# Performance work log

Measured on AMD Instinct MI355X. Metric: run time of the kernel, lower is better.

The kernel has to match this reference:

```python
import jax, jax.numpy as jnp
import numpy as np

B, T, D, H = 4, 2048, 1024, 8
d = D // H
EPS = 1e-12  # torch F.normalize eps


def _l2norm(x):
    n = jnp.sqrt(jnp.sum(x * x, axis=-1, keepdims=True))
    return x / jnp.maximum(n, EPS)


def setup_inputs() -> dict:
    key = jax.random.key(0)
    ks = jax.random.split(key, 7)
    s = 1.0 / np.sqrt(D)
    return {
        "x": jax.random.normal(ks[0], (B, T, D), dtype=jnp.float32),
        "Wq": jax.random.uniform(ks[1], (D, D), jnp.float32, -s, s),
        "Wk": jax.random.uniform(ks[2], (D, D), jnp.float32, -s, s),
        "Wv": jax.random.uniform(ks[3], (D, D), jnp.float32, -s, s),
        "Wo": jax.random.uniform(ks[4], (D, D), jnp.float32, -s, s),
        "Wlr": jax.random.uniform(ks[5], (D, D), jnp.float32, -s, s),
        "b_lr": jnp.zeros((D,), jnp.float32),
    }


def reference(x, Wq, Wk, Wv, Wo, Wlr, b_lr):
    # projections (torch Linear: y = x @ W.T)
    q = (x @ Wq.T).reshape(B, T, H, d)
    k = _l2norm((x @ Wk.T).reshape(B, T, H, d))
    v = _l2norm((x @ Wv.T).reshape(B, T, H, d))
    lr = jax.nn.sigmoid(x @ Wlr.T + b_lr).reshape(B, T, H, d)

    # scan over time; state w: [B,H,d,d]
    def step(w, qkvl):
        q_t, k_t, v_t, lr_t = qkvl  # each [B,H,d]
        v_old = jnp.einsum('bhij,bhj->bhi', w, k_t)          # retrieve
        w = w + (lr_t * (v_t - v_old))[..., :, None] * k_t[..., None, :]
        o_t = jnp.einsum('bhij,bhj->bhi', w, q_t)            # read
        return w, o_t

    to_t = lambda a: jnp.moveaxis(a, 1, 0)  # [B,T,H,d] -> [T,B,H,d]
    w0 = jnp.zeros((B, H, d, d), dtype=q.dtype)
    _, o = jax.lax.scan(step, w0, (to_t(q), to_t(k), to_t(v), to_t(lr)))
    o = jnp.moveaxis(o, 0, 1).reshape(B, T, D)
    return o @ Wo.T
```

## Files before the change

### kernel.cpp

```cpp
#include <hip/hip_runtime.h>
#include <math.h>

#define Bsz  4
#define Tlen 2048
#define Dm   1024
#define Hh   8
#define dh   128
#define Mrows (Bsz * Tlen)

typedef __attribute__((ext_vector_type(8))) short  s16x8;
typedef __attribute__((ext_vector_type(4))) float  f32x4;

#define DPP_ADD(x, ctrl) \
    ((x) + __int_as_float(__builtin_amdgcn_update_dpp( \
        0, __float_as_int(x), (ctrl), 0xf, 0xf, true)))

__device__ inline unsigned short f2b_rne(float f) {
    unsigned int u = __float_as_uint(f);
    u += 0x7FFFu + ((u >> 16) & 1u);
    return (unsigned short)(u >> 16);
}

__global__ __launch_bounds__(256) void cvt_f32_bf16(const float* __restrict__ in,
                                                    unsigned short* __restrict__ out)
{
    const size_t i = ((size_t)blockIdx.x * 256 + threadIdx.x) * 4;
    float4 v = *(const float4*)&in[i];
    ushort4 o;
    o.x = f2b_rne(v.x); o.y = f2b_rne(v.y);
    o.z = f2b_rne(v.z); o.w = f2b_rne(v.w);
    *(ushort4*)&out[i] = o;
}

__global__ __launch_bounds__(256) void gemm_bf16(const unsigned short* __restrict__ A,
                                                 const unsigned short* __restrict__ Wt,
                                                 const float* __restrict__ bias,
                                                 float* __restrict__ Y,
                                                 int mode)
{
    __shared__ __align__(16) unsigned short As[128 * 32];
    __shared__ __align__(16) unsigned short Bs[128 * 32];

    const int tid   = threadIdx.x;
    const int w     = tid >> 6;
    const int lane  = tid & 63;
    const int r4    = lane >> 2;
    const int p4    = lane & 3;
    const int row16 = lane & 15;
    const int quad  = lane >> 4;

    const int m0 = blockIdx.y * 128;
    const int n0 = blockIdx.x * 128;
    const int wm = (w >> 1) * 64;
    const int wn = (w & 1) * 64;

    f32x4 acc[4][4];
#pragma unroll
    for (int i = 0; i < 4; ++i)
#pragma unroll
        for (int j = 0; j < 4; ++j)
            acc[i][j] = (f32x4){0.f, 0.f, 0.f, 0.f};

    for (int k0 = 0; k0 < 1024; k0 += 32) {
        __syncthreads();
#pragma unroll
        for (int c = 0; c < 2; ++c) {
            const int ml  = w * 32 + c * 16 + r4;
            const int swz = (ml >> 1) & 3;
            const unsigned short* ga = A  + (size_t)(m0 + ml) * 1024 + k0 + ((p4 ^ swz) << 3);
            const unsigned short* gb = Wt + (size_t)(n0 + ml) * 1024 + k0 + ((p4 ^ swz) << 3);
            __builtin_amdgcn_global_load_lds(
                (const __attribute__((address_space(1))) void*)ga,
                (__attribute__((address_space(3))) void*)&As[(w * 32 + c * 16) * 32], 16, 0, 0);
            __builtin_amdgcn_global_load_lds(
                (const __attribute__((address_space(1))) void*)gb,
                (__attribute__((address_space(3))) void*)&Bs[(w * 32 + c * 16) * 32], 16, 0, 0);
        }
        __syncthreads();

        s16x8 af[4], bf[4];
#pragma unroll
        for (int bm = 0; bm < 4; ++bm) {
            const int ml  = wm + bm * 16 + row16;
            const int pos = quad ^ ((ml >> 1) & 3);
            af[bm] = *(const s16x8*)&As[ml * 32 + pos * 8];
        }
#pragma unroll
        for (int bn = 0; bn < 4; ++bn) {
            const int nl  = wn + bn * 16 + row16;
            const int pos = quad ^ ((nl >> 1) & 3);
            bf[bn] = *(const s16x8*)&Bs[nl * 32 + pos * 8];
        }
#pragma unroll
        for (int bm = 0; bm < 4; ++bm)
#pragma unroll
            for (int bn = 0; bn < 4; ++bn)
                acc[bm][bn] = __builtin_amdgcn_mfma_f32_16x16x32_bf16(af[bm], bf[bn], acc[bm][bn], 0, 0, 0);
    }

#pragma unroll
    for (int bm = 0; bm < 4; ++bm) {
        const int row = m0 + wm + bm * 16 + quad * 4;
#pragma unroll
        for (int bn = 0; bn < 4; ++bn) {
            const int col = n0 + wn + bn * 16 + row16;
            const float bb = bias ? bias[col] : 0.f;
#pragma unroll
            for (int r = 0; r < 4; ++r) {
                float val = acc[bm][bn][r] + bb;
                if (mode == 1) val = 1.f / (1.f + __expf(-val));
                Y[(size_t)(row + r) * 1024 + col] = val;
            }
        }
    }
}

__global__ __launch_bounds__(256) void l2norm_kq(float* __restrict__ Kb,
                                                 float* __restrict__ Vb,
                                                 const float* __restrict__ Qb,
                                                 float* __restrict__ KQ)
{
    const int gtid = blockIdx.x * 256 + threadIdx.x;
    const int row  = gtid >> 6;
    const int lane = threadIdx.x & 63;
    const size_t base = (size_t)row * dh + lane * 2;

    float2 k2 = *(float2*)&Kb[base];
    float2 v2 = *(float2*)&Vb[base];
    float2 q2 = *(const float2*)&Qb[base];
    float sk = k2.x * k2.x + k2.y * k2.y;
    float sv = v2.x * v2.x + v2.y * v2.y;
    float sq = k2.x * q2.x + k2.y * q2.y;
#pragma unroll
    for (int off = 1; off < 64; off <<= 1) {
        sk += __shfl_xor(sk, off);
        sv += __shfl_xor(sv, off);
        sq += __shfl_xor(sq, off);
    }
    const float rk = 1.f / fmaxf(sqrtf(sk), 1e-12f);
    const float rv = 1.f / fmaxf(sqrtf(sv), 1e-12f);
    k2.x *= rk; k2.y *= rk;
    v2.x *= rv; v2.y *= rv;
    *(float2*)&Kb[base] = k2;
    *(float2*)&Vb[base] = v2;
    if (lane == 0) {
        const int b = row / (Tlen * Hh);
        const int t = (row / Hh) % Tlen;
        const int h = row % Hh;
        KQ[(size_t)(b * Hh + h) * Tlen + t] = sq * rk;
    }
}

__global__ __launch_bounds__(64) void scan_kernel(const float* __restrict__ Q,
                                                  const float* __restrict__ Kb,
                                                  const float* __restrict__ Vb,
                                                  const float* __restrict__ LR,
                                                  const float* __restrict__ KQ,
                                                  unsigned short* __restrict__ Obb)
{
    const int bid = blockIdx.x;
    const int bh  = bid & 31;
    const int rg  = bid >> 5;
    const int b   = bh >> 3, h = bh & 7;
    const int lane = threadIdx.x;
    const int rl   = lane >> 4;
    const int c16  = lane & 15;
    const int row  = rg * 4 + rl;

    const size_t base = (size_t)b * Tlen * Dm + (size_t)h * dh;
    const float* kp  = Kb + base + c16 * 8;
    const float* qp  = Q  + base + c16 * 8;
    const float* vp  = Vb + base + row;
    const float* lp  = LR + base + row;
    const float* kqp = KQ + (size_t)(b * Hh + h) * Tlen;
    unsigned short* op = Obb + base + row;

    float w[8];
#pragma unroll
    for (int i = 0; i < 8; ++i) w[i] = 0.f;

    float4 kr[8][2], qr[8][2];
    float  vv[8], lv[8], kqv[8];
#pragma unroll
    for (int u = 0; u < 8; ++u) {
        const size_t off = (size_t)u * Dm;
        kr[u][0] = *(const float4*)(kp + off);
        kr[u][1] = *(const float4*)(kp + off + 4);
        qr[u][0] = *(const float4*)(qp + off);
        qr[u][1] = *(const float4*)(qp + off + 4);
        vv[u] = vp[off];
        lv[u] = lp[off];
        kqv[u] = kqp[u];
    }

    float o8[8];

    for (int t = 0; t < Tlen; t += 8) {
#pragma unroll
        for (int u = 0; u < 8; ++u) {
            const int tc = t + u;
            const float4 ka = kr[u][0], kb = kr[u][1];
            const float4 qa = qr[u][0], qb = qr[u][1];
            const float vr = vv[u], lrr = lv[u], kq = kqv[u];

            int tn = tc + 8; if (tn >= Tlen) tn = Tlen - 1;
            const size_t offn = (size_t)tn * Dm;
            kr[u][0] = *(const float4*)(kp + offn);
            kr[u][1] = *(const float4*)(kp + offn + 4);
            qr[u][0] = *(const float4*)(qp + offn);
            qr[u][1] = *(const float4*)(qp + offn + 4);
            vv[u] = vp[offn];
            lv[u] = lp[offn];
            kqv[u] = kqp[tn];

            float d1 = (fmaf(w[1], ka.y, w[0] * ka.x) + fmaf(w[3], ka.w, w[2] * ka.z)) +
                       (fmaf(w[5], kb.y, w[4] * kb.x) + fmaf(w[7], kb.w, w[6] * kb.z));
            float d2 = (fmaf(w[1], qa.y, w[0] * qa.x) + fmaf(w[3], qa.w, w[2] * qa.z)) +
                       (fmaf(w[5], qb.y, w[4] * qb.x) + fmaf(w[7], qb.w, w[6] * qb.z));

            d1 = DPP_ADD(d1, 0xB1);
            d1 = DPP_ADD(d1, 0x4E);
            d1 = DPP_ADD(d1, 0x141);
            d1 = DPP_ADD(d1, 0x140);
            const float coef = lrr * (vr - d1);

            w[0] = fmaf(coef, ka.x, w[0]); w[1] = fmaf(coef, ka.y, w[1]);
            w[2] = fmaf(coef, ka.z, w[2]); w[3] = fmaf(coef, ka.w, w[3]);
            w[4] = fmaf(coef, kb.x, w[4]); w[5] = fmaf(coef, kb.y, w[5]);
            w[6] = fmaf(coef, kb.z, w[6]); w[7] = fmaf(coef, kb.w, w[7]);

            d2 = DPP_ADD(d2, 0xB1);
            d2 = DPP_ADD(d2, 0x4E);
            d2 = DPP_ADD(d2, 0x141);
            d2 = DPP_ADD(d2, 0x140);
            o8[u] = fmaf(coef, kq, d2);
        }

        float sel = o8[0];
#pragma unroll
        for (int j = 1; j < 8; ++j)
            sel = (c16 == j) ? o8[j] : sel;
        if (c16 < 8)
            op[(size_t)(t + c16) * Dm] = f2b_rne(sel);
    }
}

extern "C" void kernel_launch(void* const* d_in, const int* in_sizes, int n_in,
                              void* d_out, int out_size, void* d_ws, size_t ws_size,
                              hipStream_t stream)
{
    const float* x    = (const float*)d_in[0];
    const float* Wq   = (const float*)d_in[1];
    const float* Wk   = (const float*)d_in[2];
    const float* Wv   = (const float*)d_in[3];
    const float* Wo   = (const float*)d_in[4];
    const float* Wlr  = (const float*)d_in[5];
    const float* b_lr = (const float*)d_in[6];

    float* ws = (float*)d_ws;
    const size_t S  = (size_t)Mrows * Dm;
    const size_t SW = (size_t)Dm * Dm;
    float* Qb  = ws;
    float* Kb  = ws + S;
    float* Vb  = ws + 2 * S;
    float* LRb = ws + 3 * S;
    unsigned short* xb  = (unsigned short*)(ws + 4 * S);
    unsigned short* Obb = xb;
    unsigned short* Wqb  = (unsigned short*)(ws + 4 * S + S / 2);
    unsigned short* Wkb  = Wqb + SW;
    unsigned short* Wvb  = Wkb + SW;
    unsigned short* Wlrb = Wvb + SW;
    unsigned short* Wob  = Wlrb + SW;
    float* KQ = (float*)(Wob + SW);

    cvt_f32_bf16<<<S / 1024, 256, 0, stream>>>(x, xb);
    cvt_f32_bf16<<<SW / 1024, 256, 0, stream>>>(Wq, Wqb);
    cvt_f32_bf16<<<SW / 1024, 256, 0, stream>>>(Wk, Wkb);
    cvt_f32_bf16<<<SW / 1024, 256, 0, stream>>>(Wv, Wvb);
    cvt_f32_bf16<<<SW / 1024, 256, 0, stream>>>(Wlr, Wlrb);
    cvt_f32_bf16<<<SW / 1024, 256, 0, stream>>>(Wo, Wob);

    dim3 gg(Dm / 128, Mrows / 128);
    gemm_bf16<<<gg, 256, 0, stream>>>(xb, Wqb, nullptr, Qb, 0);
    gemm_bf16<<<gg, 256, 0, stream>>>(xb, Wkb, nullptr, Kb, 0);
    gemm_bf16<<<gg, 256, 0, stream>>>(xb, Wvb, nullptr, Vb, 0);
    gemm_bf16<<<gg, 256, 0, stream>>>(xb, Wlrb, b_lr, LRb, 1);

    l2norm_kq<<<(Bsz * Tlen * Hh) / 4, 256, 0, stream>>>(Kb, Vb, Qb, KQ);

    scan_kernel<<<Bsz * Hh * 32, 64, 0, stream>>>(Qb, Kb, Vb, LRb, KQ, Obb);

    gemm_bf16<<<gg, 256, 0, stream>>>(Obb, Wob, nullptr, (float*)d_out, 0);
}
```

Before: 681.6 us.

## Split delta-rule scan into serial coefficient pass and chunked MFMA output

After: 638.7 us. 1.07x faster.

```diff
diff --git a/kernel.cpp b/kernel.cpp
--- a/kernel.cpp
+++ b/kernel.cpp
@@ -7,6 +7,8 @@
 #define Hh   8
 #define dh   128
 #define Mrows (Bsz * Tlen)
+#define CH   128
+#define NCH  (Tlen / CH)
 
 typedef __attribute__((ext_vector_type(8))) short  s16x8;
 typedef __attribute__((ext_vector_type(4))) float  f32x4;
@@ -14,6 +16,8 @@
 #define DPP_ADD(x, ctrl) \
     ((x) + __int_as_float(__builtin_amdgcn_update_dpp( \
         0, __float_as_int(x), (ctrl), 0xf, 0xf, true)))
+#define SWZ_ADD16(x) \
+    ((x) + __int_as_float(__builtin_amdgcn_ds_swizzle(__float_as_int(x), 0x401F)))
 
 __device__ inline unsigned short f2b_rne(float f) {
     unsigned int u = __float_as_uint(f);
@@ -35,7 +39,8 @@
 __global__ __launch_bounds__(256) void gemm_bf16(const unsigned short* __restrict__ A,
                                                  const unsigned short* __restrict__ Wt,
                                                  const float* __restrict__ bias,
-                                                 float* __restrict__ Y,
+                                                 float* __restrict__ Yf,
+                                                 unsigned short* __restrict__ Y16,
                                                  int mode)
 {
     __shared__ __align__(16) unsigned short As[128 * 32];
@@ -109,16 +114,16 @@
             for (int r = 0; r < 4; ++r) {
                 float val = acc[bm][bn][r] + bb;
                 if (mode == 1) val = 1.f / (1.f + __expf(-val));
-                Y[(size_t)(row + r) * 1024 + col] = val;
+                if (mode == 2) Y16[(size_t)(row + r) * 1024 + col] = f2b_rne(val);
+                else           Yf [(size_t)(row + r) * 1024 + col] = val;
             }
         }
     }
 }
 
-__global__ __launch_bounds__(256) void l2norm_kq(float* __restrict__ Kb,
-                                                 float* __restrict__ Vb,
-                                                 const float* __restrict__ Qb,
-                                                 float* __restrict__ KQ)
+__global__ __launch_bounds__(256) void l2norm_rows(float* __restrict__ Kb,
+                                                   float* __restrict__ Vb,
+                                                   unsigned short* __restrict__ K16)
 {
     const int gtid = blockIdx.x * 256 + threadIdx.x;
     const int row  = gtid >> 6;
@@ -127,15 +132,12 @@
 
     float2 k2 = *(float2*)&Kb[base];
     float2 v2 = *(float2*)&Vb[base];
-    float2 q2 = *(const float2*)&Qb[base];
     float sk = k2.x * k2.x + k2.y * k2.y;
     float sv = v2.x * v2.x + v2.y * v2.y;
-    float sq = k2.x * q2.x + k2.y * q2.y;
 #pragma unroll
     for (int off = 1; off < 64; off <<= 1) {
         sk += __shfl_xor(sk, off);
         sv += __shfl_xor(sv, off);
-        sq += __shfl_xor(sq, off);
     }
     const float rk = 1.f / fmaxf(sqrtf(sk), 1e-12f);
     const float rv = 1.f / fmaxf(sqrtf(sv), 1e-12f);
@@ -143,105 +145,256 @@
     v2.x *= rv; v2.y *= rv;
     *(float2*)&Kb[base] = k2;
     *(float2*)&Vb[base] = v2;
-    if (lane == 0) {
-        const int b = row / (Tlen * Hh);
-        const int t = (row / Hh) % Tlen;
-        const int h = row % Hh;
-        KQ[(size_t)(b * Hh + h) * Tlen + t] = sq * rk;
-    }
-}
-
-__global__ __launch_bounds__(64) void scan_kernel(const float* __restrict__ Q,
-                                                  const float* __restrict__ Kb,
-                                                  const float* __restrict__ Vb,
-                                                  const float* __restrict__ LR,
-                                                  const float* __restrict__ KQ,
-                                                  unsigned short* __restrict__ Obb)
+    const unsigned int pk = (unsigned int)f2b_rne(k2.x) |
+                            ((unsigned int)f2b_rne(k2.y) << 16);
+    ((unsigned int*)K16)[base >> 1] = pk;
+}
+
+__global__ __launch_bounds__(64) void scan_coef(const float* __restrict__ Kb,
+                                                const float* __restrict__ Vb,
+                                                const float* __restrict__ LR,
+                                                unsigned short* __restrict__ Ut,
+                                                unsigned short* __restrict__ Wcp)
 {
     const int bid = blockIdx.x;
     const int bh  = bid & 31;
     const int rg  = bid >> 5;
     const int b   = bh >> 3, h = bh & 7;
     const int lane = threadIdx.x;
-    const int rl   = lane >> 4;
-    const int c16  = lane & 15;
-    const int row  = rg * 4 + rl;
+    const int rl   = lane >> 5;
+    const int c32  = lane & 31;
+    const int row  = rg * 2 + rl;
 
     const size_t base = (size_t)b * Tlen * Dm + (size_t)h * dh;
-    const float* kp  = Kb + base + c16 * 8;
-    const float* qp  = Q  + base + c16 * 8;
-    const float* vp  = Vb + base + row;
-    const float* lp  = LR + base + row;
-    const float* kqp = KQ + (size_t)(b * Hh + h) * Tlen;
-    unsigned short* op = Obb + base + row;
-
-    float w[8];
-#pragma unroll
-    for (int i = 0; i < 8; ++i) w[i] = 0.f;
-
-    float4 kr[8][2], qr[8][2];
-    float  vv[8], lv[8], kqv[8];
+    const float* kp = Kb + base + c32 * 4;
+    const float* vp = Vb + base + row;
+    const float* lp = LR + base + row;
+    unsigned short* up = Ut + ((size_t)bh * dh + row) * Tlen;
+
+    float w0 = 0.f, w1 = 0.f, w2 = 0.f, w3 = 0.f;
+
+    float4 kr[8];
+    float  vv[8], lv[8];
 #pragma unroll
     for (int u = 0; u < 8; ++u) {
         const size_t off = (size_t)u * Dm;
-        kr[u][0] = *(const float4*)(kp + off);
-        kr[u][1] = *(const float4*)(kp + off + 4);
-        qr[u][0] = *(const float4*)(qp + off);
-        qr[u][1] = *(const float4*)(qp + off + 4);
+        kr[u] = *(const float4*)(kp + off);
         vv[u] = vp[off];
         lv[u] = lp[off];
-        kqv[u] = kqp[u];
     }
 
     float o8[8];
 
     for (int t = 0; t < Tlen; t += 8) {
+        if ((t & (CH - 1)) == 0) {
+            const int c = t >> 7;
+            uint2 wc;
+            wc.x = (unsigned int)f2b_rne(w0) | ((unsigned int)f2b_rne(w1) << 16);
+            wc.y = (unsigned int)f2b_rne(w2) | ((unsigned int)f2b_rne(w3) << 16);
+            *(uint2*)&Wcp[(((size_t)bh * NCH + c) * dh + row) * dh + c32 * 4] = wc;
+        }
 #pragma unroll
         for (int u = 0; u < 8; ++u) {
             const int tc = t + u;
-            const float4 ka = kr[u][0], kb = kr[u][1];
-            const float4 qa = qr[u][0], qb = qr[u][1];
-            const float vr = vv[u], lrr = lv[u], kq = kqv[u];
+            const float4 k4 = kr[u];
+            const float vr = vv[u], lrr = lv[u];
 
             int tn = tc + 8; if (tn >= Tlen) tn = Tlen - 1;
             const size_t offn = (size_t)tn * Dm;
-            kr[u][0] = *(const float4*)(kp + offn);
-            kr[u][1] = *(const float4*)(kp + offn + 4);
-            qr[u][0] = *(const float4*)(qp + offn);
-            qr[u][1] = *(const float4*)(qp + offn + 4);
+            kr[u] = *(const float4*)(kp + offn);
             vv[u] = vp[offn];
             lv[u] = lp[offn];
-            kqv[u] = kqp[tn];
-
-            float d1 = (fmaf(w[1], ka.y, w[0] * ka.x) + fmaf(w[3], ka.w, w[2] * ka.z)) +
-                       (fmaf(w[5], kb.y, w[4] * kb.x) + fmaf(w[7], kb.w, w[6] * kb.z));
-            float d2 = (fmaf(w[1], qa.y, w[0] * qa.x) + fmaf(w[3], qa.w, w[2] * qa.z)) +
-                       (fmaf(w[5], qb.y, w[4] * qb.x) + fmaf(w[7], qb.w, w[6] * qb.z));
-
+
+            float d1 = fmaf(w1, k4.y, w0 * k4.x) + fmaf(w3, k4.w, w2 * k4.z);
             d1 = DPP_ADD(d1, 0xB1);
             d1 = DPP_ADD(d1, 0x4E);
             d1 = DPP_ADD(d1, 0x141);
             d1 = DPP_ADD(d1, 0x140);
+            d1 = SWZ_ADD16(d1);
+
             const float coef = lrr * (vr - d1);
-
-            w[0] = fmaf(coef, ka.x, w[0]); w[1] = fmaf(coef, ka.y, w[1]);
-            w[2] = fmaf(coef, ka.z, w[2]); w[3] = fmaf(coef, ka.w, w[3]);
-            w[4] = fmaf(coef, kb.x, w[4]); w[5] = fmaf(coef, kb.y, w[5]);
-            w[6] = fmaf(coef, kb.z, w[6]); w[7] = fmaf(coef, kb.w, w[7]);
-
-            d2 = DPP_ADD(d2, 0xB1);
-            d2 = DPP_ADD(d2, 0x4E);
-            d2 = DPP_ADD(d2, 0x141);
-            d2 = DPP_ADD(d2, 0x140);
-            o8[u] = fmaf(coef, kq, d2);
-        }
-
-        float sel = o8[0];
-#pragma unroll
-        for (int j = 1; j < 8; ++j)
-            sel = (c16 == j) ? o8[j] : sel;
-        if (c16 < 8)
-            op[(size_t)(t + c16) * Dm] = f2b_rne(sel);
+            w0 = fmaf(coef, k4.x, w0); w1 = fmaf(coef, k4.y, w1);
+            w2 = fmaf(coef, k4.z, w2); w3 = fmaf(coef, k4.w, w3);
+            o8[u] = coef;
+        }
+        uint4 pk;
+        pk.x = (unsigned int)f2b_rne(o8[0]) | ((unsigned int)f2b_rne(o8[1]) << 16);
+        pk.y = (unsigned int)f2b_rne(o8[2]) | ((unsigned int)f2b_rne(o8[3]) << 16);
+        pk.z = (unsigned int)f2b_rne(o8[4]) | ((unsigned int)f2b_rne(o8[5]) << 16);
+        pk.w = (unsigned int)f2b_rne(o8[6]) | ((unsigned int)f2b_rne(o8[7]) << 16);
+        if (c32 == 0)
+            *(uint4*)&up[t] = pk;
+    }
+}
+
+__global__ __launch_bounds__(256) void chunk_o(const unsigned short* __restrict__ Q16,
+                                               const unsigned short* __restrict__ K16,
+                                               const unsigned short* __restrict__ Ut,
+                                               const unsigned short* __restrict__ Wcp,
+                                               unsigned short* __restrict__ Obb)
+{
+    __shared__ __align__(16) unsigned short As[128 * 32];
+    __shared__ __align__(16) unsigned short Bs[128 * 32];
+    __shared__ __align__(16) unsigned short Sb[128 * 136];
+
+    const int blk = blockIdx.x;
+    const int c   = blk & (NCH - 1);
+    const int bh  = blk >> 4;
+    const int b   = bh >> 3, h = bh & 7;
+
+    const int tid   = threadIdx.x;
+    const int w     = tid >> 6;
+    const int lane  = tid & 63;
+    const int r4    = lane >> 2;
+    const int p4    = lane & 3;
+    const int row16 = lane & 15;
+    const int quad  = lane >> 4;
+    const int wm = (w >> 1) * 64;
+    const int wn = (w & 1) * 64;
+
+    const size_t qkbase = (size_t)b * Tlen * Dm + (size_t)(c * CH) * Dm + (size_t)h * dh;
+    const size_t ubase  = (size_t)bh * dh * Tlen + (size_t)c * CH;
+    const size_t wbase  = ((size_t)bh * NCH + c) * dh * dh;
+
+    f32x4 acc[4][4];
+#pragma unroll
+    for (int i = 0; i < 4; ++i)
+#pragma unroll
+        for (int j = 0; j < 4; ++j)
+            acc[i][j] = (f32x4){0.f, 0.f, 0.f, 0.f};
+
+    for (int k0 = 0; k0 < 128; k0 += 32) {
+        __syncthreads();
+#pragma unroll
+        for (int cc = 0; cc < 2; ++cc) {
+            const int ml  = w * 32 + cc * 16 + r4;
+            const int swz = (ml >> 1) & 3;
+            const unsigned short* ga = Q16 + qkbase + (size_t)ml * Dm + k0 + ((p4 ^ swz) << 3);
+            const unsigned short* gb = K16 + qkbase + (size_t)ml * Dm + k0 + ((p4 ^ swz) << 3);
+            __builtin_amdgcn_global_load_lds(
+                (const __attribute__((address_space(1))) void*)ga,
+                (__attribute__((address_space(3))) void*)&As[(w * 32 + cc * 16) * 32], 16, 0, 0);
+            __builtin_amdgcn_global_load_lds(
+                (const __attribute__((address_space(1))) void*)gb,
+                (__attribute__((address_space(3))) void*)&Bs[(w * 32 + cc * 16) * 32], 16, 0, 0);
+        }
+        __syncthreads();
+
+        s16x8 af[4], bf[4];
+#pragma unroll
+        for (int bm = 0; bm < 4; ++bm) {
+            const int ml  = wm + bm * 16 + row16;
+            const int pos = quad ^ ((ml >> 1) & 3);
+            af[bm] = *(const s16x8*)&As[ml * 32 + pos * 8];
+        }
+#pragma unroll
+        for (int bn = 0; bn < 4; ++bn) {
+            const int nl  = wn + bn * 16 + row16;
+            const int pos = quad ^ ((nl >> 1) & 3);
+            bf[bn] = *(const s16x8*)&Bs[nl * 32 + pos * 8];
+        }
+#pragma unroll
+        for (int bm = 0; bm < 4; ++bm)
+#pragma unroll
+            for (int bn = 0; bn < 4; ++bn)
+                acc[bm][bn] = __builtin_amdgcn_mfma_f32_16x16x32_bf16(af[bm], bf[bn], acc[bm][bn], 0, 0, 0);
+    }
+
+#pragma unroll
+    for (int bm = 0; bm < 4; ++bm) {
+#pragma unroll
+        for (int bn = 0; bn < 4; ++bn) {
+            const int s_loc = wn + bn * 16 + row16;
+#pragma unroll
+            for (int r = 0; r < 4; ++r) {
+                const int t_loc = wm + bm * 16 + quad * 4 + r;
+                const float val = (s_loc <= t_loc) ? acc[bm][bn][r] : 0.f;
+                Sb[t_loc * 136 + s_loc] = f2b_rne(val);
+            }
+            acc[bm][bn] = (f32x4){0.f, 0.f, 0.f, 0.f};
+        }
+    }
+
+    for (int k0 = 0; k0 < 128; k0 += 32) {
+        __syncthreads();
+#pragma unroll
+        for (int cc = 0; cc < 2; ++cc) {
+            const int nl  = w * 32 + cc * 16 + r4;
+            const int swz = (nl >> 1) & 3;
+            const unsigned short* gb = Ut + ubase + (size_t)nl * Tlen + k0 + ((p4 ^ swz) << 3);
+            __builtin_amdgcn_global_load_lds(
+                (const __attribute__((address_space(1))) void*)gb,
+                (__attribute__((address_space(3))) void*)&Bs[(w * 32 + cc * 16) * 32], 16, 0, 0);
+        }
+        __syncthreads();
+
+        s16x8 af[4], bf[4];
+#pragma unroll
+        for (int bm = 0; bm < 4; ++bm) {
+            const int ml = wm + bm * 16 + row16;
+            af[bm] = *(const s16x8*)&Sb[ml * 136 + k0 + quad * 8];
+        }
+#pragma unroll
+        for (int bn = 0; bn < 4; ++bn) {
+            const int nl  = wn + bn * 16 + row16;
+            const int pos = quad ^ ((nl >> 1) & 3);
+            bf[bn] = *(const s16x8*)&Bs[nl * 32 + pos * 8];
+        }
+#pragma unroll
+        for (int bm = 0; bm < 4; ++bm)
+#pragma unroll
+            for (int bn = 0; bn < 4; ++bn)
+                acc[bm][bn] = __builtin_amdgcn_mfma_f32_16x16x32_bf16(af[bm], bf[bn], acc[bm][bn], 0, 0, 0);
+    }
+
+    for (int k0 = 0; k0 < 128; k0 += 32) {
+        __syncthreads();
+#pragma unroll
+        for (int cc = 0; cc < 2; ++cc) {
+            const int ml  = w * 32 + cc * 16 + r4;
+            const int swz = (ml >> 1) & 3;
+            const unsigned short* ga = Q16 + qkbase + (size_t)ml * Dm + k0 + ((p4 ^ swz) << 3);
+            const unsigned short* gb = Wcp + wbase + (size_t)ml * dh + k0 + ((p4 ^ swz) << 3);
+            __builtin_amdgcn_global_load_lds(
+                (const __attribute__((address_space(1))) void*)ga,
+                (__attribute__((address_space(3))) void*)&As[(w * 32 + cc * 16) * 32], 16, 0, 0);
+            __builtin_amdgcn_global_load_lds(
+                (const __attribute__((address_space(1))) void*)gb,
+                (__attribute__((address_space(3))) void*)&Bs[(w * 32 + cc * 16) * 32], 16, 0, 0);
+        }
+        __syncthreads();
+
+        s16x8 af[4], bf[4];
+#pragma unroll
+        for (int bm = 0; bm < 4; ++bm) {
+            const int ml  = wm + bm * 16 + row16;
+            const int pos = quad ^ ((ml >> 1) & 3);
+            af[bm] = *(const s16x8*)&As[ml * 32 + pos * 8];
+        }
+#pragma unroll
+        for (int bn = 0; bn < 4; ++bn) {
+            const int nl  = wn + bn * 16 + row16;
+            const int pos = quad ^ ((nl >> 1) & 3);
+            bf[bn] = *(const s16x8*)&Bs[nl * 32 + pos * 8];
+        }
+#pragma unroll
+        for (int bm = 0; bm < 4; ++bm)
+#pragma unroll
+            for (int bn = 0; bn < 4; ++bn)
+                acc[bm][bn] = __builtin_amdgcn_mfma_f32_16x16x32_bf16(af[bm], bf[bn], acc[bm][bn], 0, 0, 0);
+    }
+
+#pragma unroll
+    for (int bm = 0; bm < 4; ++bm) {
+#pragma unroll
+        for (int bn = 0; bn < 4; ++bn) {
+            const int i_loc = wn + bn * 16 + row16;
+#pragma unroll
+            for (int r = 0; r < 4; ++r) {
+                const int t_loc = wm + bm * 16 + quad * 4 + r;
+                Obb[qkbase + (size_t)t_loc * Dm + i_loc] = f2b_rne(acc[bm][bn][r]);
+            }
+        }
     }
 }
 
@@ -260,18 +413,20 @@
     float* ws = (float*)d_ws;
     const size_t S  = (size_t)Mrows * Dm;
     const size_t SW = (size_t)Dm * Dm;
-    float* Qb  = ws;
-    float* Kb  = ws + S;
-    float* Vb  = ws + 2 * S;
-    float* LRb = ws + 3 * S;
-    unsigned short* xb  = (unsigned short*)(ws + 4 * S);
-    unsigned short* Obb = xb;
-    unsigned short* Wqb  = (unsigned short*)(ws + 4 * S + S / 2);
+    float* Kb  = ws;
+    float* Vb  = ws + S;
+    float* LRb = ws + 2 * S;
+    unsigned short* xb   = (unsigned short*)(ws + 3 * S);
+    unsigned short* Wcp  = xb;
+    unsigned short* Q16  = xb + S;
+    unsigned short* K16  = Q16 + S;
+    unsigned short* Ut   = K16 + S;
+    unsigned short* Obb  = Ut + S;
+    unsigned short* Wqb  = Obb + S;
     unsigned short* Wkb  = Wqb + SW;
     unsigned short* Wvb  = Wkb + SW;
     unsigned short* Wlrb = Wvb + SW;
     unsigned short* Wob  = Wlrb + SW;
-    float* KQ = (float*)(Wob + SW);
 
     cvt_f32_bf16<<<S / 1024, 256, 0, stream>>>(x, xb);
     cvt_f32_bf16<<<SW / 1024, 256, 0, stream>>>(Wq, Wqb);
@@ -281,14 +436,16 @@
     cvt_f32_bf16<<<SW / 1024, 256, 0, stream>>>(Wo, Wob);
 
     dim3 gg(Dm / 128, Mrows / 128);
-    gemm_bf16<<<gg, 256, 0, stream>>>(xb, Wqb, nullptr, Qb, 0);
-    gemm_bf16<<<gg, 256, 0, stream>>>(xb, Wkb, nullptr, Kb, 0);
-    gemm_bf16<<<gg, 256, 0, stream>>>(xb, Wvb, nullptr, Vb, 0);
-    gemm_bf16<<<gg, 256, 0, stream>>>(xb, Wlrb, b_lr, LRb, 1);
-
-    l2norm_kq<<<(Bsz * Tlen * Hh) / 4, 256, 0, stream>>>(Kb, Vb, Qb, KQ);
-
-    scan_kernel<<<Bsz * Hh * 32, 64, 0, stream>>>(Qb, Kb, Vb, LRb, KQ, Obb);
-
-    gemm_bf16<<<gg, 256, 0, stream>>>(Obb, Wob, nullptr, (float*)d_out, 0);
-}
+    gemm_bf16<<<gg, 256, 0, stream>>>(xb, Wqb, nullptr, nullptr, Q16, 2);
+    gemm_bf16<<<gg, 256, 0, stream>>>(xb, Wkb, nullptr, Kb, nullptr, 0);
+    gemm_bf16<<<gg, 256, 0, stream>>>(xb, Wvb, nullptr, Vb, nullptr, 0);
+    gemm_bf16<<<gg, 256, 0, stream>>>(xb, Wlrb, b_lr, LRb, nullptr, 1);
+
+    l2norm_rows<<<(Bsz * Tlen * Hh) / 4, 256, 0, stream>>>(Kb, Vb, K16);
+
+    scan_coef<<<Bsz * Hh * 64, 64, 0, stream>>>(Kb, Vb, LRb, Ut, Wcp);
+
+    chunk_o<<<Bsz * Hh * NCH, 256, 0, stream>>>(Q16, K16, Ut, Wcp, Obb);
+
+    gemm_bf16<<<gg, 256, 0, stream>>>(Obb, Wob, nullptr, (float*)d_out, nullptr, 0);
+}
```
